# Kernel optimization log

Measured on AMD Instinct MI355X. Metric: run time of the kernel, lower is better.

## Reference

```python
import jax, jax.numpy as jnp
import numpy as np

N = 100000
E = 1600000
D = 128


def setup_inputs() -> dict:
    key = jax.random.key(0)
    ks = jax.random.split(key, 8)
    x = jax.random.normal(ks[0], (N, D), dtype=jnp.float32)
    src = jax.random.randint(ks[1], (E,), 0, N, dtype=jnp.int64)
    dst = jax.random.randint(ks[2], (E,), 0, N, dtype=jnp.int64)
    # lin_self initialized to identity (nn.init.eye_), zero-ish bias in torch default;
    # we use random params for a general correctness baseline.
    W_self = jax.random.normal(ks[3], (D, D), dtype=jnp.float32) * 0.05
    b_self = jax.random.normal(ks[4], (D,), dtype=jnp.float32) * 0.05
    W_nei = jax.random.normal(ks[5], (D, D), dtype=jnp.float32) * 0.05
    b_nei = jax.random.normal(ks[6], (D,), dtype=jnp.float32) * 0.05
    return {"x": x, "src": src, "dst": dst, "W_self": W_self, "b_self": b_self,
            "W_nei": W_nei, "b_nei": b_nei}


def reference(x, src, dst, W_self, b_self, W_nei, b_nei):
    # self path: x @ W_self.T + b_self (torch Linear convention)
    self_x = x @ W_self.T + b_self  # [N, D]
    # neighbor mean: segment-sum of gathered neighbor feats over destination node
    nei_sum = jax.ops.segment_sum(x[src], dst, num_segments=N)  # [N, D]
    deg = jax.ops.segment_sum(jnp.ones((E,), dtype=x.dtype), dst, num_segments=N)  # [N]
    has_nei = deg > 0
    nei_mean = nei_sum / jnp.maximum(deg, 1.0)[:, None]  # safe divide
    # nodes with no neighbors contribute exactly 0 (bias is NOT applied), matching
    # the torch loop which skips empty adjacency lists.
    nei_acc = jnp.where(has_nei[:, None], nei_mean @ W_nei.T + b_nei, 0.0)
    return jax.nn.relu(self_x + nei_acc)
```

## Files before the change

### kernel.cpp

```cpp
#include <hip/hip_runtime.h>

#define D 128
#define NPB 128
#define NBMAX 1024
#define TILE_E 8192
#define CAP2 2560
#define CAP2H 3584
#define BSTR2 72
#define CONV_BLOCKS 128

typedef short bf16x8 __attribute__((ext_vector_type(8)));
typedef float f32x4  __attribute__((ext_vector_type(4)));
typedef float f32x2  __attribute__((ext_vector_type(2)));

__device__ inline unsigned pack_bf2(float a, float b) {
    unsigned ua = __builtin_bit_cast(unsigned, a);
    unsigned ub = __builtin_bit_cast(unsigned, b);
    ua = (ua + 0x7FFFu + ((ua >> 16) & 1u)) >> 16;
    ub = (ub + 0x7FFFu + ((ub >> 16) & 1u)) >> 16;
    return ua | (ub << 16);
}

__global__ __launch_bounds__(1024) void zero_kernel(unsigned* __restrict__ p, int n)
{
    int i = threadIdx.x;
    if (i < n) p[i] = 0u;
}

__global__ __launch_bounds__(1024) void prep_kernel(
    const float* __restrict__ x, unsigned* __restrict__ xq, int total8,
    const float* __restrict__ Wself, const float* __restrict__ Wnei,
    unsigned short* __restrict__ wb, int w8,
    const int* __restrict__ src, const int* __restrict__ dst,
    unsigned* __restrict__ bucket_cnt, unsigned* __restrict__ edges,
    int E, int NB, int binBlocks)
{
    __shared__ unsigned lcnt[NBMAX];
    __shared__ unsigned lbase[NBMAX];
    const int tid = threadIdx.x;

    if (blockIdx.x >= binBlocks) {
        const int cb = blockIdx.x - binBlocks;
        const int stride = CONV_BLOCKS * 1024;
        const int tot = total8 + 16 + 2 * w8;
        for (int i = cb * 1024 + tid; i < tot; i += stride) {
            if (i < total8) {
                const float4* p = reinterpret_cast<const float4*>(x + (size_t)i * 8);
                float4 a = p[0], b = p[1];
                int q0 = __builtin_amdgcn_cvt_pk_fp8_f32(a.x, a.y, 0, false);
                q0     = __builtin_amdgcn_cvt_pk_fp8_f32(a.z, a.w, q0, true);
                int q1 = __builtin_amdgcn_cvt_pk_fp8_f32(b.x, b.y, 0, false);
                q1     = __builtin_amdgcn_cvt_pk_fp8_f32(b.z, b.w, q1, true);
                reinterpret_cast<uint2*>(xq)[i] = make_uint2((unsigned)q0, (unsigned)q1);
            } else if (i < total8 + 16) {
                reinterpret_cast<uint2*>(xq)[i] = make_uint2(0u, 0u);
            } else {
                const float* srcp;
                unsigned short* dstp;
                int j;
                int ib = i - 16;
                if (ib < total8 + w8) { srcp = Wself; dstp = wb;          j = ib - total8; }
                else                  { srcp = Wnei;  dstp = wb + w8 * 8; j = ib - total8 - w8; }
                const float4* p = reinterpret_cast<const float4*>(srcp + (size_t)j * 8);
                float4 a = p[0], b = p[1];
                reinterpret_cast<uint4*>(dstp)[j] =
                    make_uint4(pack_bf2(a.x, a.y), pack_bf2(a.z, a.w),
                               pack_bf2(b.x, b.y), pack_bf2(b.z, b.w));
            }
        }
        return;
    }

    const int e0 = blockIdx.x * TILE_E + tid * 8;
    int d8[8], s8[8];
    if (e0 + 8 <= E) {
        int4 a = *reinterpret_cast<const int4*>(dst + e0);
        int4 b = *reinterpret_cast<const int4*>(dst + e0 + 4);
        d8[0] = a.x; d8[1] = a.y; d8[2] = a.z; d8[3] = a.w;
        d8[4] = b.x; d8[5] = b.y; d8[6] = b.z; d8[7] = b.w;
        int4 c = *reinterpret_cast<const int4*>(src + e0);
        int4 e = *reinterpret_cast<const int4*>(src + e0 + 4);
        s8[0] = c.x; s8[1] = c.y; s8[2] = c.z; s8[3] = c.w;
        s8[4] = e.x; s8[5] = e.y; s8[6] = e.z; s8[7] = e.w;
    } else {
#pragma unroll
        for (int k = 0; k < 8; k++) {
            bool v = (e0 + k) < E;
            d8[k] = v ? dst[e0 + k] : -1;
            s8[k] = v ? src[e0 + k] : 0;
        }
    }

    for (int i = tid; i < NB; i += 1024) lcnt[i] = 0;
    __syncthreads();
#pragma unroll
    for (int k = 0; k < 8; k++)
        if (d8[k] >= 0) atomicAdd(&lcnt[((unsigned)d8[k]) >> 7], 1u);
    __syncthreads();
    for (int i = tid; i < NB; i += 1024) {
        unsigned c = lcnt[i];
        lbase[i] = c ? ((unsigned)i * CAP2 + atomicAdd(&bucket_cnt[i], c)) : 0u;
        lcnt[i] = 0;
    }
    __syncthreads();
#pragma unroll
    for (int k = 0; k < 8; k++) {
        if (d8[k] >= 0) {
            unsigned d_ = (unsigned)d8[k];
            unsigned b  = d_ >> 7;
            unsigned r  = atomicAdd(&lcnt[b], 1u);
            unsigned slot = lbase[b] + r;
            if (slot < (b + 1u) * CAP2)
                edges[slot] = ((d_ & 127u) << 20) | (unsigned)s8[k];
        }
    }
}

__global__ __launch_bounds__(512, 4) void gather_kernel(
    const unsigned char* __restrict__ xq,
    const unsigned* __restrict__ bucket_cnt,
    const unsigned* __restrict__ edges,
    unsigned short* __restrict__ nm,
    unsigned* __restrict__ deg, int Nn)
{
    __shared__ unsigned lds_src[CAP2H];
    __shared__ unsigned shc[64];
    __shared__ unsigned offs[64 + 1];
    __shared__ unsigned cursors[64];
    __shared__ unsigned tdeg[64];

    const int b   = blockIdx.x >> 1;
    const int hb  = blockIdx.x & 1;
    const int tid = threadIdx.x;
    const int n0  = b * NPB + hb * 64;
    const unsigned start = (unsigned)b * CAP2;
    unsigned cnt = bucket_cnt[b];
    if (cnt > CAP2) cnt = CAP2;

    if (tid < 64) shc[tid] = 0;
    __syncthreads();
    for (unsigned i = tid; i < cnt; i += 512) {
        unsigned node = edges[start + i] >> 20;
        if ((int)(node >> 6) == hb) atomicAdd(&shc[node & 63u], 1u);
    }
    __syncthreads();
    unsigned myc = (tid < 64) ? shc[tid] : 0u;
    unsigned pc  = (myc + 15u) & ~15u;
    if (tid < 64) shc[tid] = pc;
    __syncthreads();
    for (int off = 1; off < 64; off <<= 1) {
        unsigned v = (tid < 64 && tid >= off) ? shc[tid - off] : 0u;
        __syncthreads();
        if (tid < 64) shc[tid] += v;
        __syncthreads();
    }
    if (tid < 64) {
        unsigned ex = shc[tid] - pc;
        offs[tid] = ex;
        cursors[tid] = ex;
        tdeg[tid] = myc;
        int n = n0 + tid;
        if (n < Nn) deg[n] = myc;
    }
    if (tid == 63) offs[64] = shc[63];
    __syncthreads();
    for (unsigned i = tid; i < cnt; i += 512) {
        unsigned e = edges[start + i];
        unsigned node = e >> 20;
        if ((int)(node >> 6) == hb) {
            unsigned slot = atomicAdd(&cursors[node & 63u], 1u);
            lds_src[slot] = e & 0xFFFFFu;
        }
    }
    if (tid < 64) {
        unsigned lo = offs[tid] + myc;
        unsigned hi = offs[tid] + pc;
        for (unsigned j = lo; j < hi; j++) lds_src[j] = (unsigned)Nn;
    }
    __syncthreads();

    const int w      = tid >> 6;
    const int lane   = tid & 63;
    const int half   = lane >> 5;
    const int lane32 = lane & 31;
    const int q2     = lane32 >> 4;
    const int sub    = lane32 & 15;

#define ACCQ(u) do { \
    acc[0] += __builtin_amdgcn_cvt_pk_f32_fp8((int)(u).x, false); \
    acc[1] += __builtin_amdgcn_cvt_pk_f32_fp8((int)(u).x, true);  \
    acc[2] += __builtin_amdgcn_cvt_pk_f32_fp8((int)(u).y, false); \
    acc[3] += __builtin_amdgcn_cvt_pk_f32_fp8((int)(u).y, true);  } while (0)

    for (int jj = 0; jj < 4; jj++) {
        const int ln = w * 8 + jj * 2 + half;
        const int n  = n0 + ln;
        f32x2 acc[4] = {f32x2{0.f, 0.f}, f32x2{0.f, 0.f},
                        f32x2{0.f, 0.f}, f32x2{0.f, 0.f}};
        unsigned tc = 0;
        if (n < Nn) {
            const unsigned o = offs[ln];
            const unsigned c = offs[ln + 1] - o;
            tc = tdeg[ln];
            for (unsigned i = 0; i < c; i += 16) {
                uint2 v[8];
#pragma unroll
                for (int l = 0; l < 8; l++)
                    v[l] = *reinterpret_cast<const uint2*>(
                        xq + (size_t)lds_src[o + i + 2 * l + q2] * D + sub * 8);
#pragma unroll
                for (int l = 0; l < 8; l++) ACCQ(v[l]);
            }
        }
#pragma unroll
        for (int q = 0; q < 4; q++) {
            acc[q].x += __shfl_xor(acc[q].x, 16);
            acc[q].y += __shfl_xor(acc[q].y, 16);
        }
        if (n < Nn && lane32 < 16) {
            uint4 wv = make_uint4(0u, 0u, 0u, 0u);
            if (tc) {
                float inv = 1.0f / (float)tc;
                wv = make_uint4(pack_bf2(acc[0].x * inv, acc[0].y * inv),
                                pack_bf2(acc[1].x * inv, acc[1].y * inv),
                                pack_bf2(acc[2].x * inv, acc[2].y * inv),
                                pack_bf2(acc[3].x * inv, acc[3].y * inv));
            }
            *reinterpret_cast<uint4*>(nm + (size_t)n * D + sub * 8) = wv;
        }
    }
#undef ACCQ
}

__global__ __launch_bounds__(256) void gemm_kernel(
    const float* __restrict__ x,
    const unsigned short* __restrict__ nm,
    const unsigned short* __restrict__ wb,
    const float* __restrict__ bself, const float* __restrict__ bnei,
    const unsigned* __restrict__ deg,
    float* __restrict__ out, int Nn)
{
    __shared__ unsigned short As[64 * BSTR2];
    __shared__ unsigned short Bs[128 * BSTR2];

    const int tid  = threadIdx.x;
    const int lane = tid & 63;
    const int w    = tid >> 6;
    const int wm   = w >> 1;
    const int wn   = w & 1;
    const int n0   = blockIdx.x * 64;

    const int arow = tid >> 2;
    const int aq   = tid & 3;
    const int brow = tid >> 1;
    const int bh   = tid & 1;

    f32x4 acc[2][4];
#pragma unroll
    for (int i = 0; i < 2; i++)
#pragma unroll
        for (int j = 0; j < 4; j++) acc[i][j] = (f32x4)(0.f);

    for (int ks = 0; ks < 4; ks++) {
        {
            const int koff = (ks & 1) * 64 + aq * 16;
            const int n = n0 + arow;
            uint4 w0 = make_uint4(0u, 0u, 0u, 0u), w1 = w0;
            if (n < Nn) {
                if (ks < 2) {
                    const float4* p = reinterpret_cast<const float4*>(
                        x + (size_t)n * D + koff);
                    float4 f0 = p[0], f1 = p[1], f2 = p[2], f3 = p[3];
                    w0 = make_uint4(pack_bf2(f0.x, f0.y), pack_bf2(f0.z, f0.w),
                                    pack_bf2(f1.x, f1.y), pack_bf2(f1.z, f1.w));
                    w1 = make_uint4(pack_bf2(f2.x, f2.y), pack_bf2(f2.z, f2.w),
                                    pack_bf2(f3.x, f3.y), pack_bf2(f3.z, f3.w));
                } else {
                    const uint4* p = reinterpret_cast<const uint4*>(
                        nm + (size_t)n * D + koff);
                    w0 = p[0]; w1 = p[1];
                }
            }
            uint4* dstp = reinterpret_cast<uint4*>(&As[arow * BSTR2 + aq * 16]);
            dstp[0] = w0; dstp[1] = w1;
        }
        {
            const int koff = (ks & 1) * 64 + bh * 32;
            const unsigned short* srcB = (ks < 2) ? wb : wb + D * D;
            const uint4* p = reinterpret_cast<const uint4*>(
                srcB + (size_t)brow * D + koff);
            uint4* dstp = reinterpret_cast<uint4*>(&Bs[brow * BSTR2 + bh * 32]);
            dstp[0] = p[0]; dstp[1] = p[1]; dstp[2] = p[2]; dstp[3] = p[3];
        }
        __syncthreads();

        const int hi8 = (lane >> 4) * 8;
#pragma unroll
        for (int ksub = 0; ksub < 2; ksub++) {
            bf16x8 af[2], bf[4];
#pragma unroll
            for (int mr = 0; mr < 2; mr++)
                af[mr] = *reinterpret_cast<const bf16x8*>(
                    &As[(wm * 32 + mr * 16 + (lane & 15)) * BSTR2 + ksub * 32 + hi8]);
#pragma unroll
            for (int nr = 0; nr < 4; nr++)
                bf[nr] = *reinterpret_cast<const bf16x8*>(
                    &Bs[(wn * 64 + nr * 16 + (lane & 15)) * BSTR2 + ksub * 32 + hi8]);
#pragma unroll
            for (int mr = 0; mr < 2; mr++)
#pragma unroll
                for (int nr = 0; nr < 4; nr++)
                    acc[mr][nr] = __builtin_amdgcn_mfma_f32_16x16x32_bf16(
                        af[mr], bf[nr], acc[mr][nr], 0, 0, 0);
        }
        __syncthreads();
    }

    float bsv[4], bnv[4];
#pragma unroll
    for (int nr = 0; nr < 4; nr++) {
        int d_ = wn * 64 + nr * 16 + (lane & 15);
        bsv[nr] = bself[d_];
        bnv[nr] = bnei[d_];
    }
#pragma unroll
    for (int mr = 0; mr < 2; mr++) {
#pragma unroll
        for (int r = 0; r < 4; r++) {
            int node = n0 + wm * 32 + mr * 16 + (lane >> 4) * 4 + r;
            if (node < Nn) {
                float hd = (deg[node] > 0u) ? 1.f : 0.f;
                float* op = out + (size_t)node * D + wn * 64 + (lane & 15);
#pragma unroll
                for (int nr = 0; nr < 4; nr++) {
                    float v = acc[mr][nr][r] + bsv[nr] + hd * bnv[nr];
                    op[nr * 16] = fmaxf(v, 0.f);
                }
            }
        }
    }
}

extern "C" void kernel_launch(void* const* d_in, const int* in_sizes, int n_in,
                              void* d_out, int out_size, void* d_ws, size_t ws_size,
                              hipStream_t stream)
{
    const float* x     = (const float*)d_in[0];
    const int*   src   = (const int*)  d_in[1];
    const int*   dst   = (const int*)  d_in[2];
    const float* Wself = (const float*)d_in[3];
    const float* bself = (const float*)d_in[4];
    const float* Wnei  = (const float*)d_in[5];
    const float* bnei  = (const float*)d_in[6];
    float* out = (float*)d_out;

    const int Nn = in_sizes[0] / D;
    const int E  = in_sizes[1];
    const int NB = (Nn + NPB - 1) / NPB;

    unsigned* bucket_cnt = (unsigned*)d_ws;
    unsigned* edges      = bucket_cnt + NBMAX;
    unsigned* deg        = edges + (size_t)NB * CAP2;
    unsigned short* nm   = (unsigned short*)(deg + ((Nn + 3) & ~3));
    unsigned short* wb   = nm + (size_t)Nn * D;
    unsigned* xq         = (unsigned*)(wb + 2 * D * D);

    zero_kernel<<<1, 1024, 0, stream>>>(bucket_cnt, NBMAX);

    int total8 = (Nn * D) / 8;
    int w8 = (D * D) / 8;
    int binBlocks = (E + TILE_E - 1) / TILE_E;
    prep_kernel<<<binBlocks + CONV_BLOCKS, 1024, 0, stream>>>(
        x, xq, total8, Wself, Wnei, wb, w8,
        src, dst, bucket_cnt, edges, E, NB, binBlocks);

    gather_kernel<<<NB * 2, 512, 0, stream>>>((const unsigned char*)xq, bucket_cnt,
                                              edges, nm, deg, Nn);

    int gemmBlocks = (Nn + 63) / 64;
    gemm_kernel<<<gemmBlocks, 256, 0, stream>>>(x, nm, wb, bself, bnei, deg, out, Nn);
}
```

Before: 96.90 us.

## Fuse neighbor gather and dual GEMM into one kernel via LDS

Merges the gather kernel and the GEMM kernel into a single kernel. Each 64-node half-bucket block keeps its neighbor means in LDS (bf16) and then runs the self and neighbor MFMA GEMMs over those rows, reusing the edge-list LDS region for the x and weight tiles. This removes the global write and re-read of the bf16 neighbor-mean matrix and the degree array, plus one kernel launch. In exchange, each block reloads the full weight matrices, the GEMM is split across 8 waves with smaller per-wave tiles, and LDS use per block goes up, which can cut occupancy.

```diff
diff --git a/kernel.cpp b/kernel.cpp
--- a/kernel.cpp
+++ b/kernel.cpp
@@ -6,6 +6,7 @@
 #define TILE_E 8192
 #define CAP2 2560
 #define CAP2H 3584
+#define NMSTR 136
 #define BSTR2 72
 #define CONV_BLOCKS 128
 
@@ -116,18 +117,25 @@
     }
 }
 
-__global__ __launch_bounds__(512, 4) void gather_kernel(
+__global__ __launch_bounds__(512, 6) void gg_kernel(
     const unsigned char* __restrict__ xq,
+    const float* __restrict__ x,
+    const unsigned short* __restrict__ wb,
+    const float* __restrict__ bself, const float* __restrict__ bnei,
     const unsigned* __restrict__ bucket_cnt,
     const unsigned* __restrict__ edges,
-    unsigned short* __restrict__ nm,
-    unsigned* __restrict__ deg, int Nn)
+    float* __restrict__ out, int Nn)
 {
-    __shared__ unsigned lds_src[CAP2H];
+    __shared__ unsigned short nmT[64 * NMSTR];
+    __shared__ unsigned short uni[13824];
     __shared__ unsigned shc[64];
     __shared__ unsigned offs[64 + 1];
     __shared__ unsigned cursors[64];
     __shared__ unsigned tdeg[64];
+
+    unsigned* lds_src = reinterpret_cast<unsigned*>(uni);
+    unsigned short* As_x = uni;
+    unsigned short* Bs   = uni + 64 * BSTR2;
 
     const int b   = blockIdx.x >> 1;
     const int hb  = blockIdx.x & 1;
@@ -159,8 +167,6 @@
         offs[tid] = ex;
         cursors[tid] = ex;
         tdeg[tid] = myc;
-        int n = n0 + tid;
-        if (n < Nn) deg[n] = myc;
     }
     if (tid == 63) offs[64] = shc[63];
     __syncthreads();
@@ -179,12 +185,13 @@
     }
     __syncthreads();
 
-    const int w      = tid >> 6;
-    const int lane   = tid & 63;
-    const int half   = lane >> 5;
-    const int lane32 = lane & 31;
-    const int q2     = lane32 >> 4;
-    const int sub    = lane32 & 15;
+    {
+        const int w      = tid >> 6;
+        const int lane   = tid & 63;
+        const int half   = lane >> 5;
+        const int lane32 = lane & 31;
+        const int q2     = lane32 >> 4;
+        const int sub    = lane32 & 15;
 
 #define ACCQ(u) do { \
     acc[0] += __builtin_amdgcn_cvt_pk_f32_fp8((int)(u).x, false); \
@@ -192,16 +199,13 @@
     acc[2] += __builtin_amdgcn_cvt_pk_f32_fp8((int)(u).y, false); \
     acc[3] += __builtin_amdgcn_cvt_pk_f32_fp8((int)(u).y, true);  } while (0)
 
-    for (int jj = 0; jj < 4; jj++) {
-        const int ln = w * 8 + jj * 2 + half;
-        const int n  = n0 + ln;
-        f32x2 acc[4] = {f32x2{0.f, 0.f}, f32x2{0.f, 0.f},
-                        f32x2{0.f, 0.f}, f32x2{0.f, 0.f}};
-        unsigned tc = 0;
-        if (n < Nn) {
+        for (int jj = 0; jj < 4; jj++) {
+            const int ln = w * 8 + jj * 2 + half;
+            f32x2 acc[4] = {f32x2{0.f, 0.f}, f32x2{0.f, 0.f},
+                            f32x2{0.f, 0.f}, f32x2{0.f, 0.f}};
             const unsigned o = offs[ln];
             const unsigned c = offs[ln + 1] - o;
-            tc = tdeg[ln];
+            const unsigned tc = tdeg[ln];
             for (unsigned i = 0; i < c; i += 16) {
                 uint2 v[8];
 #pragma unroll
@@ -211,115 +215,97 @@
 #pragma unroll
                 for (int l = 0; l < 8; l++) ACCQ(v[l]);
             }
-        }
-#pragma unroll
-        for (int q = 0; q < 4; q++) {
-            acc[q].x += __shfl_xor(acc[q].x, 16);
-            acc[q].y += __shfl_xor(acc[q].y, 16);
-        }
-        if (n < Nn && lane32 < 16) {
-            uint4 wv = make_uint4(0u, 0u, 0u, 0u);
-            if (tc) {
-                float inv = 1.0f / (float)tc;
-                wv = make_uint4(pack_bf2(acc[0].x * inv, acc[0].y * inv),
-                                pack_bf2(acc[1].x * inv, acc[1].y * inv),
-                                pack_bf2(acc[2].x * inv, acc[2].y * inv),
-                                pack_bf2(acc[3].x * inv, acc[3].y * inv));
-            }
-            *reinterpret_cast<uint4*>(nm + (size_t)n * D + sub * 8) = wv;
-        }
-    }
+#pragma unroll
+            for (int q = 0; q < 4; q++) {
+                acc[q].x += __shfl_xor(acc[q].x, 16);
+                acc[q].y += __shfl_xor(acc[q].y, 16);
+            }
+            if (lane32 < 16) {
+                uint4 wv = make_uint4(0u, 0u, 0u, 0u);
+                if (tc) {
+                    float inv = 1.0f / (float)tc;
+                    wv = make_uint4(pack_bf2(acc[0].x * inv, acc[0].y * inv),
+                                    pack_bf2(acc[1].x * inv, acc[1].y * inv),
+                                    pack_bf2(acc[2].x * inv, acc[2].y * inv),
+                                    pack_bf2(acc[3].x * inv, acc[3].y * inv));
+                }
+                *reinterpret_cast<uint4*>(&nmT[ln * NMSTR + sub * 8]) = wv;
+            }
+        }
 #undef ACCQ
-}
-
-__global__ __launch_bounds__(256) void gemm_kernel(
-    const float* __restrict__ x,
-    const unsigned short* __restrict__ nm,
-    const unsigned short* __restrict__ wb,
-    const float* __restrict__ bself, const float* __restrict__ bnei,
-    const unsigned* __restrict__ deg,
-    float* __restrict__ out, int Nn)
-{
-    __shared__ unsigned short As[64 * BSTR2];
-    __shared__ unsigned short Bs[128 * BSTR2];
-
-    const int tid  = threadIdx.x;
+    }
+    __syncthreads();
+
     const int lane = tid & 63;
     const int w    = tid >> 6;
-    const int wm   = w >> 1;
-    const int wn   = w & 1;
-    const int n0   = blockIdx.x * 64;
-
-    const int arow = tid >> 2;
-    const int aq   = tid & 3;
-    const int brow = tid >> 1;
-    const int bh   = tid & 1;
-
-    f32x4 acc[2][4];
+    const int wm   = w >> 2;
+    const int wn   = w & 3;
+
+    f32x4 acc2[2][2];
 #pragma unroll
     for (int i = 0; i < 2; i++)
 #pragma unroll
-        for (int j = 0; j < 4; j++) acc[i][j] = (f32x4)(0.f);
+        for (int j = 0; j < 2; j++) acc2[i][j] = (f32x4)(0.f);
+
+    const int axrow = tid >> 3;
+    const int axoct = tid & 7;
+    const int brow  = tid >> 2;
+    const int bq    = tid & 3;
 
     for (int ks = 0; ks < 4; ks++) {
+        if (ks < 2) {
+            const int n = n0 + axrow;
+            uint4 w0 = make_uint4(0u, 0u, 0u, 0u);
+            if (n < Nn) {
+                const float4* p = reinterpret_cast<const float4*>(
+                    x + (size_t)n * D + ks * 64 + axoct * 8);
+                float4 f0 = p[0], f1 = p[1];
+                w0 = make_uint4(pack_bf2(f0.x, f0.y), pack_bf2(f0.z, f0.w),
+                                pack_bf2(f1.x, f1.y), pack_bf2(f1.z, f1.w));
+            }
+            *reinterpret_cast<uint4*>(&As_x[axrow * BSTR2 + axoct * 8]) = w0;
+        }
         {
-            const int koff = (ks & 1) * 64 + aq * 16;
-            const int n = n0 + arow;
-            uint4 w0 = make_uint4(0u, 0u, 0u, 0u), w1 = w0;
-            if (n < Nn) {
-                if (ks < 2) {
-                    const float4* p = reinterpret_cast<const float4*>(
-                        x + (size_t)n * D + koff);
-                    float4 f0 = p[0], f1 = p[1], f2 = p[2], f3 = p[3];
-                    w0 = make_uint4(pack_bf2(f0.x, f0.y), pack_bf2(f0.z, f0.w),
-                                    pack_bf2(f1.x, f1.y), pack_bf2(f1.z, f1.w));
-                    w1 = make_uint4(pack_bf2(f2.x, f2.y), pack_bf2(f2.z, f2.w),
-                                    pack_bf2(f3.x, f3.y), pack_bf2(f3.z, f3.w));
-                } else {
-                    const uint4* p = reinterpret_cast<const uint4*>(
-                        nm + (size_t)n * D + koff);
-                    w0 = p[0]; w1 = p[1];
-                }
-            }
-            uint4* dstp = reinterpret_cast<uint4*>(&As[arow * BSTR2 + aq * 16]);
-            dstp[0] = w0; dstp[1] = w1;
-        }
-        {
-            const int koff = (ks & 1) * 64 + bh * 32;
+            const int koff = (ks & 1) * 64 + bq * 16;
             const unsigned short* srcB = (ks < 2) ? wb : wb + D * D;
             const uint4* p = reinterpret_cast<const uint4*>(
                 srcB + (size_t)brow * D + koff);
-            uint4* dstp = reinterpret_cast<uint4*>(&Bs[brow * BSTR2 + bh * 32]);
-            dstp[0] = p[0]; dstp[1] = p[1]; dstp[2] = p[2]; dstp[3] = p[3];
+            uint4* dstp = reinterpret_cast<uint4*>(&Bs[brow * BSTR2 + bq * 16]);
+            dstp[0] = p[0]; dstp[1] = p[1];
         }
         __syncthreads();
 
         const int hi8 = (lane >> 4) * 8;
 #pragma unroll
         for (int ksub = 0; ksub < 2; ksub++) {
-            bf16x8 af[2], bf[4];
+            bf16x8 af[2], bf[2];
+#pragma unroll
+            for (int mr = 0; mr < 2; mr++) {
+                const int row = wm * 32 + mr * 16 + (lane & 15);
+                af[mr] = (ks < 2)
+                    ? *reinterpret_cast<const bf16x8*>(
+                          &As_x[row * BSTR2 + ksub * 32 + hi8])
+                    : *reinterpret_cast<const bf16x8*>(
+                          &nmT[row * NMSTR + (ks - 2) * 64 + ksub * 32 + hi8]);
+            }
+#pragma unroll
+            for (int nr = 0; nr < 2; nr++)
+                bf[nr] = *reinterpret_cast<const bf16x8*>(
+                    &Bs[(wn * 32 + nr * 16 + (lane & 15)) * BSTR2 + ksub * 32 + hi8]);
 #pragma unroll
             for (int mr = 0; mr < 2; mr++)
-                af[mr] = *reinterpret_cast<const bf16x8*>(
-                    &As[(wm * 32 + mr * 16 + (lane & 15)) * BSTR2 + ksub * 32 + hi8]);
-#pragma unroll
-            for (int nr = 0; nr < 4; nr++)
-                bf[nr] = *reinterpret_cast<const bf16x8*>(
-                    &Bs[(wn * 64 + nr * 16 + (lane & 15)) * BSTR2 + ksub * 32 + hi8]);
-#pragma unroll
-            for (int mr = 0; mr < 2; mr++)
-#pragma unroll
-                for (int nr = 0; nr < 4; nr++)
-                    acc[mr][nr] = __builtin_amdgcn_mfma_f32_16x16x32_bf16(
-                        af[mr], bf[nr], acc[mr][nr], 0, 0, 0);
+#pragma unroll
+                for (int nr = 0; nr < 2; nr++)
+                    acc2[mr][nr] = __builtin_amdgcn_mfma_f32_16x16x32_bf16(
+                        af[mr], bf[nr], acc2[mr][nr], 0, 0, 0);
         }
         __syncthreads();
     }
 
-    float bsv[4], bnv[4];
-#pragma unroll
-    for (int nr = 0; nr < 4; nr++) {
-        int d_ = wn * 64 + nr * 16 + (lane & 15);
+    float bsv[2], bnv[2];
+#pragma unroll
+    for (int nr = 0; nr < 2; nr++) {
+        int d_ = wn * 32 + nr * 16 + (lane & 15);
         bsv[nr] = bself[d_];
         bnv[nr] = bnei[d_];
     }
@@ -327,13 +313,14 @@
     for (int mr = 0; mr < 2; mr++) {
 #pragma unroll
         for (int r = 0; r < 4; r++) {
-            int node = n0 + wm * 32 + mr * 16 + (lane >> 4) * 4 + r;
+            int ln = wm * 32 + mr * 16 + (lane >> 4) * 4 + r;
+            int node = n0 + ln;
             if (node < Nn) {
-                float hd = (deg[node] > 0u) ? 1.f : 0.f;
-                float* op = out + (size_t)node * D + wn * 64 + (lane & 15);
-#pragma unroll
-                for (int nr = 0; nr < 4; nr++) {
-                    float v = acc[mr][nr][r] + bsv[nr] + hd * bnv[nr];
+                float hd = (tdeg[ln] > 0u) ? 1.f : 0.f;
+                float* op = out + (size_t)node * D + wn * 32 + (lane & 15);
+#pragma unroll
+                for (int nr = 0; nr < 2; nr++) {
+                    float v = acc2[mr][nr][r] + bsv[nr] + hd * bnv[nr];
                     op[nr * 16] = fmaxf(v, 0.f);
                 }
             }
@@ -360,9 +347,7 @@
 
     unsigned* bucket_cnt = (unsigned*)d_ws;
     unsigned* edges      = bucket_cnt + NBMAX;
-    unsigned* deg        = edges + (size_t)NB * CAP2;
-    unsigned short* nm   = (unsigned short*)(deg + ((Nn + 3) & ~3));
-    unsigned short* wb   = nm + (size_t)Nn * D;
+    unsigned short* wb   = (unsigned short*)(edges + (size_t)NB * CAP2);
     unsigned* xq         = (unsigned*)(wb + 2 * D * D);
 
     zero_kernel<<<1, 1024, 0, stream>>>(bucket_cnt, NBMAX);
@@ -374,9 +359,7 @@
         x, xq, total8, Wself, Wnei, wb, w8,
         src, dst, bucket_cnt, edges, E, NB, binBlocks);
 
-    gather_kernel<<<NB * 2, 512, 0, stream>>>((const unsigned char*)xq, bucket_cnt,
-                                              edges, nm, deg, Nn);
-
-    int gemmBlocks = (Nn + 63) / 64;
-    gemm_kernel<<<gemmBlocks, 256, 0, stream>>>(x, nm, wb, bself, bnei, deg, out, Nn);
-}
+    gg_kernel<<<NB * 2, 512, 0, stream>>>((const unsigned char*)xq, x, wb,
+                                          bself, bnei, bucket_cnt, edges,
+                                          out, Nn);
+}
```

Measured after the change: 88.68 us. 1.09x faster.
